# Optimization experiments

Hardware: AMD Instinct MI355X
Metric: run time of the kernel (lower is better)

Reference implementation:

```python
import jax, jax.numpy as jnp
import numpy as np
from jax import lax

EPS = 1e-5

# ---- 1-bit activation quantizer with straight-through estimator ----
@jax.custom_vjp
def ste_sign(x):
    return jnp.sign(x)

def _ste_sign_fwd(x):
    return jnp.sign(x), x

def _ste_sign_bwd(res, g):
    x = res
    # clipped STE: pass gradient where |x| <= 1
    return (g * (jnp.abs(x) <= 1.0).astype(g.dtype),)

ste_sign.defvjp(_ste_sign_fwd, _ste_sign_bwd)

# ---- 1-bit weight binarization: sign(w) * per-out-channel mean(|w|), STE ----
@jax.custom_vjp
def bin_weight(w):
    alpha = jnp.mean(jnp.abs(w), axis=(1, 2, 3), keepdims=True)  # [O,1,1,1]
    return jnp.sign(w) * alpha

def _bw_fwd(w):
    return bin_weight(w), w

def _bw_bwd(res, g):
    w = res
    # weight_clip=1: straight-through inside the clip range
    return (g * (jnp.abs(w) <= 1.0).astype(g.dtype),)

bin_weight.defvjp(_bw_fwd, _bw_bwd)

def conv3x3(x, w):
    # zero padding=1, stride=1, NCHW / OIHW
    return lax.conv_general_dilated(
        x, w, window_strides=(1, 1), padding=((1, 1), (1, 1)),
        dimension_numbers=('NCHW', 'OIHW', 'NCHW'))

def batchnorm(x, gamma, beta):
    # training-mode BN with batch statistics over (N,H,W)
    mean = jnp.mean(x, axis=(0, 2, 3), keepdims=True)
    var = jnp.var(x, axis=(0, 2, 3), keepdims=True)
    xn = (x - mean) * lax.rsqrt(var + EPS)
    return xn * gamma[None, :, None, None] + beta[None, :, None, None]


def setup_inputs() -> dict:
    key = jax.random.key(0)
    k1, k2, k3 = jax.random.split(key, 3)
    N, C, H, W = 32, 256, 56, 56
    return {
        'x': jax.random.normal(k1, (N, C, H, W), dtype=jnp.float32),
        'w1': jax.random.normal(k2, (C, C, 3, 3), dtype=jnp.float32) * 0.05,
        'gamma1': jnp.ones((C,), dtype=jnp.float32),
        'beta1': jnp.zeros((C,), dtype=jnp.float32),
        'w2': jax.random.normal(k3, (C, C, 3, 3), dtype=jnp.float32) * 0.05,
        'gamma2': jnp.ones((C,), dtype=jnp.float32),
        'beta2': jnp.zeros((C,), dtype=jnp.float32),
    }


def reference(x, w1, gamma1, beta1, w2, gamma2, beta2):
    identity = x
    out = ste_sign(x)                       # quantized activation (1-bit, signed)
    out = conv3x3(out, bin_weight(w1))      # BinConv 3x3, stride 1
    out = batchnorm(out, gamma1, beta1)
    out = ste_sign(out)
    out = conv3x3(out, bin_weight(w2))
    out = batchnorm(out, gamma2, beta2)
    return out + identity                   # residual add (downsample=None)
```

## Files before the change

### kernel.cpp

```cpp
#include <hip/hip_runtime.h>
#include <stdint.h>

#define NB 32
#define CH 256
#define HH 56
#define WW 56
#define HWSZ (HH*WW)
#define NPIX (NB*HWSZ)
#define NTAPS 9
#define KKE (CH*NTAPS)
#define NPIXD 100352.0
#define WQ_CONV (NTAPS*8*8*64*16)
#define HSTRIDE 272

typedef int int4v  __attribute__((ext_vector_type(4)));
typedef int int16v __attribute__((ext_vector_type(16)));

__global__ void init_kernel(long long* __restrict__ sums8) {
    int t = blockIdx.x*256 + threadIdx.x;
    if (t < 2*8*512) sums8[t] = 0;
}

__global__ void wqpack_kernel(const float* __restrict__ w1, const float* __restrict__ w2,
                              int8_t* __restrict__ wq) {
    int t = blockIdx.x*256 + threadIdx.x;
    int conv = blockIdx.y;
    const float* w = conv ? w2 : w1;
    int lane = t & 63;
    int g = t >> 6;
    int nb = g & 7, h = g >> 3;
    int ks = h & 7, tap = h >> 3;
    int o = nb*32 + (lane & 31);
    int cin0 = ks*32 + (lane >> 5)*16;
    int wd[4];
    #pragma unroll
    for (int q = 0; q < 4; ++q) {
        int wv = 0;
        #pragma unroll
        for (int j = 0; j < 4; ++j) {
            float v = w[(size_t)(o*CH + cin0 + q*4 + j)*NTAPS + tap];
            int s = (v > 0.f) ? 1 : ((v < 0.f) ? -1 : 0);
            wv |= (s & 0xff) << (8*j);
        }
        wd[q] = wv;
    }
    *(int4v*)(wq + (size_t)conv*WQ_CONV + (size_t)t*16) = (int4v){wd[0], wd[1], wd[2], wd[3]};
}

__global__ void alpha_kernel(const float* __restrict__ w1, const float* __restrict__ w2,
                             float* __restrict__ alpha) {
    int o = blockIdx.x; int conv = blockIdx.y;
    const float* w = conv ? w2 : w1;
    float s = 0.f;
    for (int i = threadIdx.x; i < KKE; i += 256) s += fabsf(w[(size_t)o*KKE + i]);
    for (int off = 32; off; off >>= 1) s += __shfl_down(s, off);
    __shared__ float l[4];
    int lane = threadIdx.x & 63, wv = threadIdx.x >> 6;
    if (lane == 0) l[wv] = s;
    __syncthreads();
    if (threadIdx.x == 0) alpha[conv*CH + o] = (l[0]+l[1]+l[2]+l[3]) * (1.f/KKE);
}

#define AOFF(IT) (((((IT)>>3)/3)*10 + (((IT)>>3)%3))*HSTRIDE + ((IT)&7)*32)

#define CONV_BODY \
    __syncthreads(); \
    int lane = t & 63; \
    int nbp = __builtin_amdgcn_readfirstlane(t >> 6); \
    int kh = lane >> 5, lr = lane & 31; \
    int r0 = lr >> 3, c0 = lr & 7; \
    int base0 = (r0*10 + c0)*HSTRIDE + kh*16; \
    int base1 = base0 + 40*HSTRIDE; \
    const int8_t* wp0 = wq + nbp*2048 + lane*16; \
    const int8_t* wp1 = wp0 + 1024; \
    int16v acc00, acc01, acc10, acc11; \
    _Pragma("unroll") \
    for (int i = 0; i < 16; ++i) { acc00[i]=0; acc01[i]=0; acc10[i]=0; acc11[i]=0; } \
    _Pragma("unroll") \
    for (int it = 0; it < 72; ++it) { \
        int4v a0 = *(const int4v*)&halo[base0 + AOFF(it)]; \
        int4v a1 = *(const int4v*)&halo[base1 + AOFF(it)]; \
        int4v b0 = *(const int4v*)(wp0 + it*8192); \
        int4v b1 = *(const int4v*)(wp1 + it*8192); \
        acc00 = __builtin_amdgcn_mfma_i32_32x32x32_i8(a0, b0, acc00, 0,0,0); \
        acc01 = __builtin_amdgcn_mfma_i32_32x32x32_i8(a0, b1, acc01, 0,0,0); \
        acc10 = __builtin_amdgcn_mfma_i32_32x32x32_i8(a1, b0, acc10, 0,0,0); \
        acc11 = __builtin_amdgcn_mfma_i32_32x32x32_i8(a1, b1, acc11, 0,0,0); \
    } \
    { \
        int s1a = 0, s2a = 0, s1b = 0, s2b = 0; \
        _Pragma("unroll") \
        for (int reg = 0; reg < 16; ++reg) { \
            int row_ = (reg & 3) + 8*(reg >> 2) + 4*kh; \
            _Pragma("unroll") \
            for (int m = 0; m < 2; ++m) { \
                int pm_ = m*32 + row_; \
                int rr_ = pm_ >> 3, cc_ = pm_ & 7; \
                size_t pbase_ = (size_t)((n0*HH + ty*8 + rr_)*WW + tx*8 + cc_)*CH; \
                int v0 = (m ? acc10[reg] : acc00[reg]); \
                int v1 = (m ? acc11[reg] : acc01[reg]); \
                cnt[pbase_ + (nbp*2+0)*32 + lr] = (int16_t)v0; \
                cnt[pbase_ + (nbp*2+1)*32 + lr] = (int16_t)v1; \
                s1a += v0; s2a += v0*v0; s1b += v1; s2b += v1*v1; \
            } \
        } \
        s1a += __shfl_down(s1a, 32); s2a += __shfl_down(s2a, 32); \
        s1b += __shfl_down(s1b, 32); s2b += __shfl_down(s2b, 32); \
        if (lane < 32) { \
            long long* sp = sums8 + (size_t)(b & 7)*512; \
            int ch0 = nbp*64 + lr, ch1 = ch0 + 32; \
            atomicAdd((unsigned long long*)&sp[2*ch0],   (unsigned long long)(long long)s1a); \
            atomicAdd((unsigned long long*)&sp[2*ch0+1], (unsigned long long)(long long)s2a); \
            atomicAdd((unsigned long long*)&sp[2*ch1],   (unsigned long long)(long long)s1b); \
            atomicAdd((unsigned long long*)&sp[2*ch1+1], (unsigned long long)(long long)s2b); \
        } \
    }

__global__ __launch_bounds__(256, 3) void conv_kernel(
        const float* __restrict__ x, const int8_t* __restrict__ wq,
        int16_t* __restrict__ cnt, long long* __restrict__ sums8) {
    __shared__ __attribute__((aligned(16))) int8_t halo[100*HSTRIDE];
    int b = blockIdx.x;
    int tile = b % 49, n0 = b / 49;
    int ty = tile / 7, tx = tile % 7;
    int t = threadIdx.x;

    if (t < 100) {
        int pix = t;
        int dr = pix / 10, dc = pix - dr*10;
        int hi = ty*8 + dr - 1, wi = tx*8 + dc - 1;
        int4v* dst = (int4v*)&halo[pix*HSTRIDE];
        if ((unsigned)hi < (unsigned)HH && (unsigned)wi < (unsigned)WW) {
            const float* xb = x + (size_t)n0*CH*HWSZ + hi*WW + wi;
            #pragma unroll 2
            for (int c16 = 0; c16 < 16; ++c16) {
                int wd[4];
                #pragma unroll
                for (int q = 0; q < 4; ++q) {
                    int wv = 0;
                    #pragma unroll
                    for (int j = 0; j < 4; ++j) {
                        float v = xb[(size_t)(c16*16 + q*4 + j)*HWSZ];
                        int s = (v > 0.f) ? 1 : ((v < 0.f) ? -1 : 0);
                        wv |= (s & 0xff) << (8*j);
                    }
                    wd[q] = wv;
                }
                dst[c16] = (int4v){wd[0], wd[1], wd[2], wd[3]};
            }
        } else {
            int4v z = {0,0,0,0};
            #pragma unroll
            for (int c16 = 0; c16 < 16; ++c16) dst[c16] = z;
        }
    }
    CONV_BODY
}

__global__ __launch_bounds__(256, 3) void conv2_kernel(
        const int16_t* __restrict__ src16, const float* __restrict__ ab,
        const int8_t* __restrict__ wq,
        int16_t* __restrict__ cnt, long long* __restrict__ sums8) {
    __shared__ __attribute__((aligned(16))) int8_t halo[100*HSTRIDE];
    int b = blockIdx.x;
    int tile = b % 49, n0 = b / 49;
    int ty = tile / 7, tx = tile % 7;
    int t = threadIdx.x;

    {
        int c16s = t & 15;
        #pragma unroll 1
        for (int k = 0; k < 7; ++k) {
            int pix = (t >> 4) + k*16;
            if (pix < 100) {
                int dr = pix / 10, dc = pix - dr*10;
                int hi = ty*8 + dr - 1, wi = tx*8 + dc - 1;
                int4v outv = {0,0,0,0};
                if ((unsigned)hi < (unsigned)HH && (unsigned)wi < (unsigned)WW) {
                    const int16_t* sp = src16 + ((size_t)(n0*HH + hi)*WW + wi)*CH + c16s*16;
                    int4v u0 = *(const int4v*)sp;
                    int4v u1 = *(const int4v*)(sp + 8);
                    int wd[4];
                    #pragma unroll
                    for (int q = 0; q < 4; ++q) {
                        int wv = 0;
                        #pragma unroll
                        for (int j = 0; j < 4; ++j) {
                            int e = q*4 + j;
                            int word = (e < 8) ? u0[e >> 1] : u1[(e-8) >> 1];
                            int sval = (e & 1) ? (word >> 16) : ((word << 16) >> 16);
                            int ch = c16s*16 + e;
                            float v = fmaf(ab[ch], (float)sval, ab[CH + ch]);
                            int s = (v > 0.f) ? 1 : ((v < 0.f) ? -1 : 0);
                            wv |= (s & 0xff) << (8*j);
                        }
                        wd[q] = wv;
                    }
                    outv = (int4v){wd[0], wd[1], wd[2], wd[3]};
                }
                *(int4v*)&halo[pix*HSTRIDE + c16s*16] = outv;
            }
        }
    }
    CONV_BODY
}

__global__ void bncoef_kernel(const long long* __restrict__ sums8,
                              const float* __restrict__ alpha,
                              const float* __restrict__ gamma, const float* __restrict__ beta,
                              float* __restrict__ ab) {
    int o = threadIdx.x;
    long long S1i = 0, S2i = 0;
    #pragma unroll
    for (int k = 0; k < 8; ++k) {
        S1i += sums8[(size_t)k*512 + 2*o];
        S2i += sums8[(size_t)k*512 + 2*o + 1];
    }
    double S1 = (double)S1i, S2 = (double)S2i;
    double mean = S1 / NPIXD;
    double var  = S2 / NPIXD - mean*mean;
    double al   = (double)alpha[o];
    double rs   = 1.0 / sqrt(al*al*var + 1e-5);
    double a    = (double)gamma[o] * al * rs;
    ab[o]      = (float)a;
    ab[CH + o] = (float)((double)beta[o] - a*mean);
}

__global__ __launch_bounds__(256) void final_kernel(const int16_t* __restrict__ cnt,
        const float* __restrict__ x, const float* __restrict__ ab, float* __restrict__ out) {
    __shared__ int4v lsd4[64*32];
    int8_t* lb = (int8_t*)lsd4;
    int b = blockIdx.x;
    int n = b / 49, tile = b - n*49;
    int p0 = tile * 64;
    int t = threadIdx.x;
    const int4v* src = (const int4v*)(cnt + ((size_t)n*HWSZ + p0)*CH);
    #pragma unroll
    for (int j = 0; j < 8; ++j) {
        int c = t + j*256;
        int pix = c >> 5, c16 = c & 31;
        *(int4v*)&lb[pix*512 + ((c16*16) ^ ((pix & 15) << 4))] = src[c];
    }
    __syncthreads();
    int pixL = t & 63;
    int cb = (t >> 6) * 64;
    #pragma unroll 1
    for (int i = 0; i < 8; ++i) {
        int ch0 = cb + i*8;
        int4v v = *(const int4v*)&lb[pixL*512 + ((ch0*2) ^ ((pixL & 15) << 4))];
        #pragma unroll
        for (int j = 0; j < 8; ++j) {
            int ch = ch0 + j;
            int word = v[j >> 1];
            int sval = (j & 1) ? (word >> 16) : ((word << 16) >> 16);
            size_t g = (size_t)(n*CH + ch)*HWSZ + p0 + pixL;
            out[g] = fmaf(ab[ch], (float)sval, ab[CH + ch]) + x[g];
        }
    }
}

extern "C" void kernel_launch(void* const* d_in, const int* in_sizes, int n_in,
                              void* d_out, int out_size, void* d_ws, size_t ws_size,
                              hipStream_t stream) {
    const float* x  = (const float*)d_in[0];
    const float* w1 = (const float*)d_in[1];
    const float* g1 = (const float*)d_in[2];
    const float* b1 = (const float*)d_in[3];
    const float* w2 = (const float*)d_in[4];
    const float* g2 = (const float*)d_in[5];
    const float* b2 = (const float*)d_in[6];
    float* out = (float*)d_out;

    char* ws = (char*)d_ws;
    size_t off = 0;
    auto alloc = [&](size_t nbytes) { char* pp = ws + off; off = (off + nbytes + 255) & ~(size_t)255; return pp; };
    int16_t*  cnt1  = (int16_t*)alloc((size_t)NPIX*CH*2);
    int16_t*  cnt2  = (int16_t*)alloc((size_t)NPIX*CH*2);
    int8_t*   wq    = (int8_t*)alloc((size_t)2*WQ_CONV);
    float*    alpha = (float*)alloc((size_t)2*CH*4);
    long long* sums8 = (long long*)alloc((size_t)2*8*512*8);
    float*    ab    = (float*)alloc((size_t)2*2*CH*4);

    init_kernel<<<32, 256, 0, stream>>>(sums8);
    wqpack_kernel<<<dim3(144, 2), 256, 0, stream>>>(w1, w2, wq);
    alpha_kernel<<<dim3(CH, 2), 256, 0, stream>>>(w1, w2, alpha);

    conv_kernel<<<1568, 256, 0, stream>>>(x, wq, cnt1, sums8);
    bncoef_kernel<<<1, CH, 0, stream>>>(sums8, alpha, g1, b1, ab);

    conv2_kernel<<<1568, 256, 0, stream>>>(cnt1, ab, wq + WQ_CONV, cnt2, sums8 + 8*512);
    bncoef_kernel<<<1, CH, 0, stream>>>(sums8 + 8*512, alpha + CH, g2, b2, ab + 2*CH);

    final_kernel<<<1568, 256, 0, stream>>>(cnt2, x, ab + 2*CH, out);
}
```

Measured before the change: 288.6 us.

## Pre-pack sign(x) into padded int8 NHWC and software-pipeline conv MFMA loads

Adds a pack_x kernel that binarizes x once into a zero-padded int8 NHWC buffer, so conv1 fills its halo with coalesced 16-byte copies instead of 100 threads doing strided float gathers. The MFMA inner loop in both convs now uses inline-asm LDS and buffer loads in a three-deep register ring, issuing loads two iterations ahead under explicit waitcnt. The aim is to hide load latency behind MFMAs and to remove the serial halo-build stall. In exchange it adds an extra launch plus an intermediate buffer round trip through memory, and more registers per thread for the ring buffers.

```diff
diff --git a/kernel.cpp b/kernel.cpp
--- a/kernel.cpp
+++ b/kernel.cpp
@@ -7,6 +7,9 @@
 #define WW 56
 #define HWSZ (HH*WW)
 #define NPIX (NB*HWSZ)
+#define HP 58
+#define WP 58
+#define PADPIX (NB*HP*WP)
 #define NTAPS 9
 #define KKE (CH*NTAPS)
 #define NPIXD 100352.0
@@ -15,6 +18,7 @@
 
 typedef int int4v  __attribute__((ext_vector_type(4)));
 typedef int int16v __attribute__((ext_vector_type(16)));
+typedef unsigned int uint4v __attribute__((ext_vector_type(4)));
 
 __global__ void init_kernel(long long* __restrict__ sums8) {
     int t = blockIdx.x*256 + threadIdx.x;
@@ -61,7 +65,51 @@
     if (threadIdx.x == 0) alpha[conv*CH + o] = (l[0]+l[1]+l[2]+l[3]) * (1.f/KKE);
 }
 
+__global__ void pack_x_kernel(const float* __restrict__ x, int8_t* __restrict__ apad) {
+    int p = blockIdx.x*256 + threadIdx.x;
+    if (p >= PADPIX) return;
+    int n  = p / (HP*WP);
+    int r  = p - n*(HP*WP);
+    int hp = r / WP, wp = r - hp*WP;
+    int4v* dst = (int4v*)(apad + (size_t)p*CH);
+    if (hp >= 1 && hp <= HH && wp >= 1 && wp <= WW) {
+        const float* xb = x + (size_t)n*CH*HWSZ + (hp-1)*WW + (wp-1);
+        #pragma unroll 2
+        for (int c16 = 0; c16 < 16; ++c16) {
+            int wd[4];
+            #pragma unroll
+            for (int q = 0; q < 4; ++q) {
+                int wv = 0;
+                #pragma unroll
+                for (int j = 0; j < 4; ++j) {
+                    float v = xb[(size_t)(c16*16 + q*4 + j)*HWSZ];
+                    int s = (v > 0.f) ? 1 : ((v < 0.f) ? -1 : 0);
+                    wv |= (s & 0xff) << (8*j);
+                }
+                wd[q] = wv;
+            }
+            dst[c16] = (int4v){wd[0], wd[1], wd[2], wd[3]};
+        }
+    } else {
+        int4v z = {0,0,0,0};
+        #pragma unroll
+        for (int c16 = 0; c16 < 16; ++c16) dst[c16] = z;
+    }
+}
+
 #define AOFF(IT) (((((IT)>>3)/3)*10 + (((IT)>>3)%3))*HSTRIDE + ((IT)&7)*32)
+
+#define ISSUE_SET(IT) do { \
+        int k_ = (IT) % 3; \
+        uint32_t ao_ = (uint32_t)AOFF(IT); \
+        uint32_t vo_ = voff + (uint32_t)(IT)*8192u; \
+        asm volatile("ds_read_b128 %0, %1" : "=v"(as_[k_][0]) : "v"(a0addr + ao_)); \
+        asm volatile("ds_read_b128 %0, %1" : "=v"(as_[k_][1]) : "v"(a1addr + ao_)); \
+        asm volatile("buffer_load_dwordx4 %0, %1, %2, 0 offen" \
+                     : "=v"(bs_[k_][0]) : "v"(vo_), "s"(rsrc)); \
+        asm volatile("buffer_load_dwordx4 %0, %1, %2, 0 offen offset:1024" \
+                     : "=v"(bs_[k_][1]) : "v"(vo_), "s"(rsrc)); \
+    } while (0)
 
 #define CONV_BODY \
     __syncthreads(); \
@@ -71,21 +119,30 @@
     int r0 = lr >> 3, c0 = lr & 7; \
     int base0 = (r0*10 + c0)*HSTRIDE + kh*16; \
     int base1 = base0 + 40*HSTRIDE; \
-    const int8_t* wp0 = wq + nbp*2048 + lane*16; \
-    const int8_t* wp1 = wp0 + 1024; \
+    uint32_t a0addr = (uint32_t)(uintptr_t)halo + (uint32_t)base0; \
+    uint32_t a1addr = (uint32_t)(uintptr_t)halo + (uint32_t)base1; \
+    uint32_t voff = (uint32_t)(nbp*2048 + lane*16); \
+    uint4v rsrc; \
+    { union { const int8_t* p; unsigned long long u; } pu_; pu_.p = wq; \
+      rsrc.x = (unsigned)pu_.u; rsrc.y = (unsigned)(pu_.u >> 32); \
+      rsrc.z = 0xffffffffu; rsrc.w = 0x00020000u; } \
+    int4v as_[3][2], bs_[3][2]; \
     int16v acc00, acc01, acc10, acc11; \
     _Pragma("unroll") \
     for (int i = 0; i < 16; ++i) { acc00[i]=0; acc01[i]=0; acc10[i]=0; acc11[i]=0; } \
+    ISSUE_SET(0); \
+    ISSUE_SET(1); \
     _Pragma("unroll") \
     for (int it = 0; it < 72; ++it) { \
-        int4v a0 = *(const int4v*)&halo[base0 + AOFF(it)]; \
-        int4v a1 = *(const int4v*)&halo[base1 + AOFF(it)]; \
-        int4v b0 = *(const int4v*)(wp0 + it*8192); \
-        int4v b1 = *(const int4v*)(wp1 + it*8192); \
-        acc00 = __builtin_amdgcn_mfma_i32_32x32x32_i8(a0, b0, acc00, 0,0,0); \
-        acc01 = __builtin_amdgcn_mfma_i32_32x32x32_i8(a0, b1, acc01, 0,0,0); \
-        acc10 = __builtin_amdgcn_mfma_i32_32x32x32_i8(a1, b0, acc10, 0,0,0); \
-        acc11 = __builtin_amdgcn_mfma_i32_32x32x32_i8(a1, b1, acc11, 0,0,0); \
+        if (it + 1 < 72) { asm volatile("s_waitcnt lgkmcnt(2) vmcnt(2)"); } \
+        else             { asm volatile("s_waitcnt lgkmcnt(0) vmcnt(0)"); } \
+        __builtin_amdgcn_sched_barrier(0); \
+        if (it + 2 < 72) { ISSUE_SET(it + 2); } \
+        int kc_ = it % 3; \
+        acc00 = __builtin_amdgcn_mfma_i32_32x32x32_i8(as_[kc_][0], bs_[kc_][0], acc00, 0,0,0); \
+        acc01 = __builtin_amdgcn_mfma_i32_32x32x32_i8(as_[kc_][0], bs_[kc_][1], acc01, 0,0,0); \
+        acc10 = __builtin_amdgcn_mfma_i32_32x32x32_i8(as_[kc_][1], bs_[kc_][0], acc10, 0,0,0); \
+        acc11 = __builtin_amdgcn_mfma_i32_32x32x32_i8(as_[kc_][1], bs_[kc_][1], acc11, 0,0,0); \
     } \
     { \
         int s1a = 0, s2a = 0, s1b = 0, s2b = 0; \
@@ -117,7 +174,7 @@
     }
 
 __global__ __launch_bounds__(256, 3) void conv_kernel(
-        const float* __restrict__ x, const int8_t* __restrict__ wq,
+        const int8_t* __restrict__ apad, const int8_t* __restrict__ wq,
         int16_t* __restrict__ cnt, long long* __restrict__ sums8) {
     __shared__ __attribute__((aligned(16))) int8_t halo[100*HSTRIDE];
     int b = blockIdx.x;
@@ -125,33 +182,15 @@
     int ty = tile / 7, tx = tile % 7;
     int t = threadIdx.x;
 
-    if (t < 100) {
-        int pix = t;
-        int dr = pix / 10, dc = pix - dr*10;
-        int hi = ty*8 + dr - 1, wi = tx*8 + dc - 1;
-        int4v* dst = (int4v*)&halo[pix*HSTRIDE];
-        if ((unsigned)hi < (unsigned)HH && (unsigned)wi < (unsigned)WW) {
-            const float* xb = x + (size_t)n0*CH*HWSZ + hi*WW + wi;
-            #pragma unroll 2
-            for (int c16 = 0; c16 < 16; ++c16) {
-                int wd[4];
-                #pragma unroll
-                for (int q = 0; q < 4; ++q) {
-                    int wv = 0;
-                    #pragma unroll
-                    for (int j = 0; j < 4; ++j) {
-                        float v = xb[(size_t)(c16*16 + q*4 + j)*HWSZ];
-                        int s = (v > 0.f) ? 1 : ((v < 0.f) ? -1 : 0);
-                        wv |= (s & 0xff) << (8*j);
-                    }
-                    wd[q] = wv;
-                }
-                dst[c16] = (int4v){wd[0], wd[1], wd[2], wd[3]};
-            }
-        } else {
-            int4v z = {0,0,0,0};
-            #pragma unroll
-            for (int c16 = 0; c16 < 16; ++c16) dst[c16] = z;
+    #pragma unroll 1
+    for (int j = 0; j < 7; ++j) {
+        int idx = t + j*256;
+        if (idx < 1600) {
+            int pix = idx >> 4, c16 = idx & 15;
+            int dr = pix / 10, dc = pix - dr*10;
+            const int4v* src = (const int4v*)(apad +
+                ((size_t)((n0*HP + ty*8+dr)*WP + tx*8+dc))*CH + c16*16);
+            *(int4v*)&halo[pix*HSTRIDE + c16*16] = *src;
         }
     }
     CONV_BODY
@@ -274,6 +313,7 @@
     char* ws = (char*)d_ws;
     size_t off = 0;
     auto alloc = [&](size_t nbytes) { char* pp = ws + off; off = (off + nbytes + 255) & ~(size_t)255; return pp; };
+    int8_t*   apad  = (int8_t*)alloc((size_t)PADPIX*CH);
     int16_t*  cnt1  = (int16_t*)alloc((size_t)NPIX*CH*2);
     int16_t*  cnt2  = (int16_t*)alloc((size_t)NPIX*CH*2);
     int8_t*   wq    = (int8_t*)alloc((size_t)2*WQ_CONV);
@@ -284,8 +324,9 @@
     init_kernel<<<32, 256, 0, stream>>>(sums8);
     wqpack_kernel<<<dim3(144, 2), 256, 0, stream>>>(w1, w2, wq);
     alpha_kernel<<<dim3(CH, 2), 256, 0, stream>>>(w1, w2, alpha);
-
-    conv_kernel<<<1568, 256, 0, stream>>>(x, wq, cnt1, sums8);
+    pack_x_kernel<<<(PADPIX + 255)/256, 256, 0, stream>>>(x, apad);
+
+    conv_kernel<<<1568, 256, 0, stream>>>(apad, wq, cnt1, sums8);
     bncoef_kernel<<<1, CH, 0, stream>>>(sums8, alpha, g1, b1, ab);
 
     conv2_kernel<<<1568, 256, 0, stream>>>(cnt1, ab, wq + WQ_CONV, cnt2, sums8 + 8*512);
```

Result: faster. 237.6 us (median of 2 runs) (-17.6%).
